# Performance work log

Hardware: AMD Instinct MI355X
Metric: run time of the kernel (lower is better)

The kernel has to match this reference:

```python
import jax, jax.numpy as jnp
import numpy as np

N = 1_000_000          # number of points
V = 65536              # number of voxels / groups (static stand-in for unique(coors))
IN_CH = 64             # 3 xyz + 61 extra features
HID = 64               # feat_channels = [64, 64]
REL_HID = 16           # rel_mlp_hidden_dims = [16]
XYZ_NORM = jnp.asarray([1.0, 1.0, 1.0], dtype=jnp.float32)
REL_DIST_SCALER = jnp.float32(1.0)


def setup_inputs() -> dict:
    key = jax.random.key(0)
    ks = jax.random.split(key, 10)

    def lin(k, i, o):
        return (jax.random.normal(k, (i, o), jnp.float32) / np.sqrt(i)).astype(jnp.float32)

    return {
        "points_xyzs": jax.random.normal(ks[0], (N, 3), jnp.float32),
        "points_feat": jax.random.normal(ks[1], (N, IN_CH - 3), jnp.float32),
        "f_cluster": jax.random.normal(ks[2], (N, 3), jnp.float32),
        "coors": jax.random.randint(ks[3], (N,), 0, V, jnp.int32),
        # rel_mlp: Linear(3,16)+BN+ReLU, Linear(16,64)+BN+ReLU (inference BN folded to scale/shift)
        "rel_w0": lin(ks[4], 3, REL_HID),
        "rel_g0": jnp.ones((REL_HID,), jnp.float32),
        "rel_b0": jnp.zeros((REL_HID,), jnp.float32),
        "rel_w1": lin(ks[5], REL_HID, IN_CH),
        "rel_g1": jnp.ones((IN_CH,), jnp.float32),
        "rel_b1": jnp.zeros((IN_CH,), jnp.float32),
        # vfe layer 0: Linear(64,64)+BN+ReLU;  vfe layer 1: Linear(128,64)+BN+ReLU (in_filters*=2 for i>0)
        "vfe_w0": lin(ks[6], IN_CH, HID),
        "vfe_g0": jnp.ones((HID,), jnp.float32),
        "vfe_b0": jnp.zeros((HID,), jnp.float32),
        "vfe_w1": lin(ks[7], 2 * HID, HID),
        "vfe_g1": jnp.ones((HID,), jnp.float32),
        "vfe_b1": jnp.zeros((HID,), jnp.float32),
    }


def _bn_relu(x, g, b):
    # inference BatchNorm1d folded into per-channel scale/shift, then ReLU
    return jax.nn.relu(x * g + b)


def _forward(points_xyzs, points_feat, f_cluster, coors,
             rel_w0, rel_g0, rel_b0, rel_w1, rel_g1, rel_b1,
             vfe_w0, vfe_g0, vfe_b0, vfe_w1, vfe_g1, vfe_b1):
    xyz = points_xyzs / XYZ_NORM                              # [N, 3]
    feats = jnp.concatenate([xyz, points_feat], axis=-1)      # [N, IN_CH]
    shortcut = feats
    fc = f_cluster / REL_DIST_SCALER                          # [N, 3]
    # relative-position MLP gating: features *= rel_mlp(f_cluster)
    h = _bn_relu(fc @ rel_w0, rel_g0, rel_b0)                 # [N, REL_HID]
    gate = _bn_relu(h @ rel_w1, rel_g1, rel_b1)               # [N, IN_CH]
    feats = feats * gate
    # VFE layer 0: per-point MLP -> voxel-wise scatter max -> gather back -> concat
    p0 = _bn_relu(feats @ vfe_w0, vfe_g0, vfe_b0)             # [N, HID]
    v0 = jax.ops.segment_max(p0, coors, num_segments=V)       # [V, HID]
    v0 = jnp.where(jnp.isfinite(v0), v0, jnp.float32(0.0))    # empty voxels -> 0
    feats = jnp.concatenate([p0, v0[coors]], axis=-1)         # [N, 2*HID]
    # VFE layer 1 (last): per-point MLP, plus residual shortcut (shapes match)
    p1 = _bn_relu(feats @ vfe_w1, vfe_g1, vfe_b1)             # [N, HID]
    return p1 + shortcut


def reference(points_xyzs, points_feat, f_cluster, coors,
              rel_w0, rel_g0, rel_b0, rel_w1, rel_g1, rel_b1,
              vfe_w0, vfe_g0, vfe_b0, vfe_w1, vfe_g1, vfe_b1):
    return _forward(points_xyzs, points_feat, f_cluster, coors,
                    rel_w0, rel_g0, rel_b0, rel_w1, rel_g1, rel_b1,
                    vfe_w0, vfe_g0, vfe_b0, vfe_w1, vfe_g1, vfe_b1)
```

## Files before the change

### kernel.cpp

```cpp
#include <hip/hip_runtime.h>
#include <hip/hip_bf16.h>


#define VVOX 65536

__global__ void __launch_bounds__(256)
sir_k1(const float* __restrict__ xyz,
       const float* __restrict__ pfeat,
       const float* __restrict__ fclu,
       const int* __restrict__ coors,
       const float* __restrict__ rw0,
       const float* __restrict__ rg0,
       const float* __restrict__ rb0,
       const float* __restrict__ rw1,
       const float* __restrict__ rg1,
       const float* __restrict__ rb1,
       const float* __restrict__ vw0,
       const float* __restrict__ vg0,
       const float* __restrict__ vb0,
       unsigned int* __restrict__ vmax,
       float* __restrict__ p0out,
       int npts)
{
    __shared__ float s_w0[48];
    __shared__ float s_b0[16];
    __shared__ float s_w1t[1024];
    __shared__ float s_b1[64];
    __shared__ float s_vw0[4096];
    __shared__ float s_vb0[64];

    const int t = threadIdx.x;
    for (int i = t; i < 48; i += 256) s_w0[i] = rw0[i] * rg0[i & 15];
    if (t < 16) s_b0[t] = rb0[t];
    for (int i = t; i < 1024; i += 256) {
        int k = i >> 4, j = i & 15;
        s_w1t[i] = rw1[j * 64 + k] * rg1[k];
    }
    if (t < 64) s_b1[t] = rb1[t];
    for (int i = t; i < 4096; i += 256) s_vw0[i] = vw0[i] * vg0[i & 63];
    if (t < 64) s_vb0[t] = vb0[t];
    __syncthreads();

    const int pt = blockIdx.x * 256 + t;
    if (pt >= npts) return;

    float f[64];
    {
        const float* xr = xyz + (size_t)pt * 3;
        f[0] = xr[0]; f[1] = xr[1]; f[2] = xr[2];
        const float* fr = pfeat + (size_t)pt * 61;
        #pragma unroll
        for (int k = 0; k < 61; ++k) f[3 + k] = fr[k];
    }

    const float* cr = fclu + (size_t)pt * 3;
    const float c0 = cr[0], c1 = cr[1], c2 = cr[2];
    float h[16];
    #pragma unroll
    for (int j = 0; j < 16; ++j) {
        float v = s_b0[j];
        v = fmaf(c0, s_w0[j], v);
        v = fmaf(c1, s_w0[16 + j], v);
        v = fmaf(c2, s_w0[32 + j], v);
        h[j] = fmaxf(v, 0.f);
    }

    float acc[64];
    #pragma unroll
    for (int c = 0; c < 64; ++c) acc[c] = s_vb0[c];

    for (int k = 0; k < 64; ++k) {
        float g = s_b1[k];
        const float* w1k = s_w1t + k * 16;
        #pragma unroll
        for (int j = 0; j < 16; ++j) g = fmaf(h[j], w1k[j], g);
        g = fmaxf(g, 0.f);
        const float gk = f[k] * g;
        const float* wk = s_vw0 + k * 64;
        #pragma unroll
        for (int c = 0; c < 64; ++c) acc[c] = fmaf(gk, wk[c], acc[c]);
    }

    const int vox = coors[pt];
    unsigned int* vrow = vmax + (size_t)vox * 64;
    const uint4* vrow4 = reinterpret_cast<const uint4*>(vrow);
    float4* orow = reinterpret_cast<float4*>(p0out + (size_t)pt * 64);
    #pragma unroll
    for (int q = 0; q < 16; ++q) {
        const uint4 cur = vrow4[q];
        float4 u;
        u.x = fmaxf(acc[q * 4 + 0], 0.f);
        u.y = fmaxf(acc[q * 4 + 1], 0.f);
        u.z = fmaxf(acc[q * 4 + 2], 0.f);
        u.w = fmaxf(acc[q * 4 + 3], 0.f);
        orow[q] = u;
        if (__float_as_uint(u.x) > cur.x) atomicMax(vrow + q * 4 + 0, __float_as_uint(u.x));
        if (__float_as_uint(u.y) > cur.y) atomicMax(vrow + q * 4 + 1, __float_as_uint(u.y));
        if (__float_as_uint(u.z) > cur.z) atomicMax(vrow + q * 4 + 2, __float_as_uint(u.z));
        if (__float_as_uint(u.w) > cur.w) atomicMax(vrow + q * 4 + 3, __float_as_uint(u.w));
    }
}

__global__ void __launch_bounds__(256)
sir_k2(const float* __restrict__ xyz,
       const float* __restrict__ pfeat,
       const int* __restrict__ coors,
       const float* __restrict__ vw1,
       const float* __restrict__ vg1,
       const float* __restrict__ vb1,
       const float* __restrict__ vmaxf,
       float* __restrict__ io,
       int npts)
{
    __shared__ float s_w[8192];
    __shared__ float s_b[64];
    const int t = threadIdx.x;
    for (int i = t; i < 8192; i += 256) s_w[i] = vw1[i] * vg1[i & 63];
    if (t < 64) s_b[t] = vb1[t];
    __syncthreads();

    const int pt = blockIdx.x * 256 + t;
    if (pt >= npts) return;

    float acc[64];
    #pragma unroll
    for (int c = 0; c < 64; ++c) acc[c] = s_b[c];

    const float4* prow = reinterpret_cast<const float4*>(io + (size_t)pt * 64);
    for (int q = 0; q < 16; ++q) {
        const float4 u = prow[q];
        const float pv[4] = { u.x, u.y, u.z, u.w };
        const float* wk = s_w + q * 4 * 64;
        #pragma unroll
        for (int i = 0; i < 4; ++i) {
            const float pk = pv[i];
            #pragma unroll
            for (int c = 0; c < 64; ++c) acc[c] = fmaf(pk, wk[i * 64 + c], acc[c]);
        }
    }

    const int vox = coors[pt];
    const float4* vrow = reinterpret_cast<const float4*>(vmaxf + (size_t)vox * 64);
    for (int q = 0; q < 16; ++q) {
        const float4 u = vrow[q];
        const float vv[4] = { u.x, u.y, u.z, u.w };
        const float* wk = s_w + (64 + q * 4) * 64;
        #pragma unroll
        for (int i = 0; i < 4; ++i) {
            const float vk = vv[i];
            #pragma unroll
            for (int c = 0; c < 64; ++c) acc[c] = fmaf(vk, wk[i * 64 + c], acc[c]);
        }
    }

    const float* xr = xyz + (size_t)pt * 3;
    const float* fr = pfeat + (size_t)pt * 61;
    float4* orow = reinterpret_cast<float4*>(io + (size_t)pt * 64);
    #pragma unroll
    for (int q = 0; q < 16; ++q) {
        float4 u;
        const int c = q * 4;
        const float s0 = (c + 0 < 3) ? xr[c + 0] : fr[c - 3];
        const float s1 = (c + 1 < 3) ? xr[c + 1] : fr[c - 2];
        const float s2 = (c + 2 < 3) ? xr[c + 2] : fr[c - 1];
        const float s3 = (c + 3 < 3) ? xr[c + 3] : fr[c + 0];
        u.x = fmaxf(acc[c + 0], 0.f) + s0;
        u.y = fmaxf(acc[c + 1], 0.f) + s1;
        u.z = fmaxf(acc[c + 2], 0.f) + s2;
        u.w = fmaxf(acc[c + 3], 0.f) + s3;
        orow[q] = u;
    }
}

extern "C" void kernel_launch(void* const* d_in, const int* in_sizes, int n_in,
                              void* d_out, int out_size, void* d_ws, size_t ws_size,
                              hipStream_t stream) {
    const float* xyz   = (const float*)d_in[0];
    const float* pfeat = (const float*)d_in[1];
    const float* fclu  = (const float*)d_in[2];
    const int*   coors = (const int*)d_in[3];
    const float* rw0 = (const float*)d_in[4];
    const float* rg0 = (const float*)d_in[5];
    const float* rb0 = (const float*)d_in[6];
    const float* rw1 = (const float*)d_in[7];
    const float* rg1 = (const float*)d_in[8];
    const float* rb1 = (const float*)d_in[9];
    const float* vw0 = (const float*)d_in[10];
    const float* vg0 = (const float*)d_in[11];
    const float* vb0 = (const float*)d_in[12];
    const float* vw1 = (const float*)d_in[13];
    const float* vg1 = (const float*)d_in[14];
    const float* vb1 = (const float*)d_in[15];

    float*        out  = (float*)d_out;
    unsigned int* vmax = (unsigned int*)d_ws;
    const int npts = in_sizes[3];
    const int blocks = (npts + 255) / 256;

    hipMemsetAsync(d_ws, 0, (size_t)VVOX * 64 * sizeof(float), stream);

    hipLaunchKernelGGL(sir_k1, dim3(blocks), dim3(256), 0, stream,
                       xyz, pfeat, fclu, coors,
                       rw0, rg0, rb0, rw1, rg1, rb1,
                       vw0, vg0, vb0, vmax, out, npts);

    hipLaunchKernelGGL(sir_k2, dim3(blocks), dim3(256), 0, stream,
                       xyz, pfeat, coors,
                       vw1, vg1, vb1, (const float*)d_ws, out, npts);
}
```

Baseline: 1.670 ms.

## Split gate and VFE0 GEMM kernels, register-block 4 points x 16 channels

The fused first kernel is split into two. One kernel computes the rel-MLP gated features and writes them into the output buffer. The second kernel runs the 64x64 projection plus the scatter-max, with each thread computing 4 points by 16 output channels and prefetching the next float4 of inputs. The second VFE kernel is restructured into the same 4x16 register tile. The aim is to cut per-thread register pressure from the 64-wide accumulator and feature arrays, and to reuse each shared-memory weight read across four points. In exchange the gated features make an extra round trip through global memory, and there is one more kernel launch.

```diff
diff --git a/kernel.cpp b/kernel.cpp
--- a/kernel.cpp
+++ b/kernel.cpp
@@ -1,57 +1,38 @@
 #include <hip/hip_runtime.h>
-#include <hip/hip_bf16.h>
 
 
 #define VVOX 65536
 
 __global__ void __launch_bounds__(256)
-sir_k1(const float* __restrict__ xyz,
-       const float* __restrict__ pfeat,
-       const float* __restrict__ fclu,
-       const int* __restrict__ coors,
-       const float* __restrict__ rw0,
-       const float* __restrict__ rg0,
-       const float* __restrict__ rb0,
-       const float* __restrict__ rw1,
-       const float* __restrict__ rg1,
-       const float* __restrict__ rb1,
-       const float* __restrict__ vw0,
-       const float* __restrict__ vg0,
-       const float* __restrict__ vb0,
-       unsigned int* __restrict__ vmax,
-       float* __restrict__ p0out,
-       int npts)
+sir_k1a(const float* __restrict__ xyz,
+        const float* __restrict__ pfeat,
+        const float* __restrict__ fclu,
+        const float* __restrict__ rw0,
+        const float* __restrict__ rg0,
+        const float* __restrict__ rb0,
+        const float* __restrict__ rw1,
+        const float* __restrict__ rg1,
+        const float* __restrict__ rb1,
+        float* __restrict__ G,
+        int npts)
 {
     __shared__ float s_w0[48];
     __shared__ float s_b0[16];
     __shared__ float s_w1t[1024];
     __shared__ float s_b1[64];
-    __shared__ float s_vw0[4096];
-    __shared__ float s_vb0[64];
 
     const int t = threadIdx.x;
-    for (int i = t; i < 48; i += 256) s_w0[i] = rw0[i] * rg0[i & 15];
+    if (t < 48) s_w0[t] = rw0[t] * rg0[t & 15];
     if (t < 16) s_b0[t] = rb0[t];
     for (int i = t; i < 1024; i += 256) {
         int k = i >> 4, j = i & 15;
         s_w1t[i] = rw1[j * 64 + k] * rg1[k];
     }
     if (t < 64) s_b1[t] = rb1[t];
-    for (int i = t; i < 4096; i += 256) s_vw0[i] = vw0[i] * vg0[i & 63];
-    if (t < 64) s_vb0[t] = vb0[t];
     __syncthreads();
 
     const int pt = blockIdx.x * 256 + t;
     if (pt >= npts) return;
-
-    float f[64];
-    {
-        const float* xr = xyz + (size_t)pt * 3;
-        f[0] = xr[0]; f[1] = xr[1]; f[2] = xr[2];
-        const float* fr = pfeat + (size_t)pt * 61;
-        #pragma unroll
-        for (int k = 0; k < 61; ++k) f[3 + k] = fr[k];
-    }
 
     const float* cr = fclu + (size_t)pt * 3;
     const float c0 = cr[0], c1 = cr[1], c2 = cr[2];
@@ -65,39 +46,120 @@
         h[j] = fmaxf(v, 0.f);
     }
 
-    float acc[64];
-    #pragma unroll
-    for (int c = 0; c < 64; ++c) acc[c] = s_vb0[c];
-
-    for (int k = 0; k < 64; ++k) {
-        float g = s_b1[k];
-        const float* w1k = s_w1t + k * 16;
-        #pragma unroll
-        for (int j = 0; j < 16; ++j) g = fmaf(h[j], w1k[j], g);
-        g = fmaxf(g, 0.f);
-        const float gk = f[k] * g;
-        const float* wk = s_vw0 + k * 64;
-        #pragma unroll
-        for (int c = 0; c < 64; ++c) acc[c] = fmaf(gk, wk[c], acc[c]);
-    }
-
-    const int vox = coors[pt];
-    unsigned int* vrow = vmax + (size_t)vox * 64;
-    const uint4* vrow4 = reinterpret_cast<const uint4*>(vrow);
-    float4* orow = reinterpret_cast<float4*>(p0out + (size_t)pt * 64);
-    #pragma unroll
-    for (int q = 0; q < 16; ++q) {
-        const uint4 cur = vrow4[q];
-        float4 u;
-        u.x = fmaxf(acc[q * 4 + 0], 0.f);
-        u.y = fmaxf(acc[q * 4 + 1], 0.f);
-        u.z = fmaxf(acc[q * 4 + 2], 0.f);
-        u.w = fmaxf(acc[q * 4 + 3], 0.f);
-        orow[q] = u;
-        if (__float_as_uint(u.x) > cur.x) atomicMax(vrow + q * 4 + 0, __float_as_uint(u.x));
-        if (__float_as_uint(u.y) > cur.y) atomicMax(vrow + q * 4 + 1, __float_as_uint(u.y));
-        if (__float_as_uint(u.z) > cur.z) atomicMax(vrow + q * 4 + 2, __float_as_uint(u.z));
-        if (__float_as_uint(u.w) > cur.w) atomicMax(vrow + q * 4 + 3, __float_as_uint(u.w));
+    const float* xr = xyz + (size_t)pt * 3;
+    const float* fr = pfeat + (size_t)pt * 61;
+    float4* Grow = reinterpret_cast<float4*>(G + (size_t)pt * 64);
+
+    #pragma unroll 4
+    for (int k4 = 0; k4 < 16; ++k4) {
+        float u[4];
+        #pragma unroll
+        for (int kk = 0; kk < 4; ++kk) {
+            const int k = k4 * 4 + kk;
+            const float* w1k = s_w1t + k * 16;
+            float g0 = s_b1[k], g1 = 0.f, g2 = 0.f, g3 = 0.f;
+            #pragma unroll
+            for (int j = 0; j < 4; ++j) {
+                g0 = fmaf(h[j],      w1k[j],      g0);
+                g1 = fmaf(h[4 + j],  w1k[4 + j],  g1);
+                g2 = fmaf(h[8 + j],  w1k[8 + j],  g2);
+                g3 = fmaf(h[12 + j], w1k[12 + j], g3);
+            }
+            const float g = fmaxf((g0 + g1) + (g2 + g3), 0.f);
+            const float fk = (k < 3) ? xr[k] : fr[k - 3];
+            u[kk] = fk * g;
+        }
+        float4 uu;
+        uu.x = u[0]; uu.y = u[1]; uu.z = u[2]; uu.w = u[3];
+        Grow[k4] = uu;
+    }
+}
+
+__global__ void __launch_bounds__(256)
+sir_k1b(const float* __restrict__ G,
+        const int* __restrict__ coors,
+        const float* __restrict__ vw0,
+        const float* __restrict__ vg0,
+        const float* __restrict__ vb0,
+        unsigned int* __restrict__ vmax,
+        float* __restrict__ p0out,
+        int npts)
+{
+    __shared__ float s_w[4096];
+    __shared__ float s_b[64];
+    const int t = threadIdx.x;
+    for (int i = t; i < 4096; i += 256) s_w[i] = vw0[i] * vg0[i & 63];
+    if (t < 64) s_b[t] = vb0[t];
+    __syncthreads();
+
+    const int cg = t & 3;
+    const int ps = t >> 2;
+    const int base = blockIdx.x * 256;
+
+    int p[4]; bool ok[4];
+    const float4* Gp[4];
+    #pragma unroll
+    for (int i = 0; i < 4; ++i) {
+        p[i] = base + ps + 64 * i;
+        ok[i] = p[i] < npts;
+        const int pc = ok[i] ? p[i] : 0;
+        Gp[i] = reinterpret_cast<const float4*>(G + (size_t)pc * 64);
+    }
+
+    float acc[4][16];
+    #pragma unroll
+    for (int i = 0; i < 4; ++i)
+        #pragma unroll
+        for (int c = 0; c < 16; ++c) acc[i][c] = s_b[cg * 16 + c];
+
+    float4 gv[4], gvn[4];
+    #pragma unroll
+    for (int i = 0; i < 4; ++i) gv[i] = Gp[i][0];
+
+    for (int k4 = 0; k4 < 16; ++k4) {
+        const int k4n = (k4 + 1) & 15;
+        #pragma unroll
+        for (int i = 0; i < 4; ++i) gvn[i] = Gp[i][k4n];
+        const float* wb = s_w + k4 * 256 + cg * 16;
+        #pragma unroll
+        for (int kk = 0; kk < 4; ++kk) {
+            const float* wr = wb + kk * 64;
+            #pragma unroll
+            for (int i = 0; i < 4; ++i) {
+                const float ga[4] = { gv[i].x, gv[i].y, gv[i].z, gv[i].w };
+                const float gk = ga[kk];
+                #pragma unroll
+                for (int c = 0; c < 16; ++c)
+                    acc[i][c] = fmaf(gk, wr[c], acc[i][c]);
+            }
+        }
+        #pragma unroll
+        for (int i = 0; i < 4; ++i) gv[i] = gvn[i];
+    }
+
+    __syncthreads();
+
+    #pragma unroll
+    for (int i = 0; i < 4; ++i) {
+        if (!ok[i]) continue;
+        const int vox = coors[p[i]];
+        unsigned int* vrow = vmax + (size_t)vox * 64 + cg * 16;
+        const uint4* vrow4 = reinterpret_cast<const uint4*>(vrow);
+        float4* orow = reinterpret_cast<float4*>(p0out + (size_t)p[i] * 64 + cg * 16);
+        #pragma unroll
+        for (int q = 0; q < 4; ++q) {
+            const uint4 cur = vrow4[q];
+            float4 u;
+            u.x = fmaxf(acc[i][q * 4 + 0], 0.f);
+            u.y = fmaxf(acc[i][q * 4 + 1], 0.f);
+            u.z = fmaxf(acc[i][q * 4 + 2], 0.f);
+            u.w = fmaxf(acc[i][q * 4 + 3], 0.f);
+            orow[q] = u;
+            if (__float_as_uint(u.x) > cur.x) atomicMax(vrow + q * 4 + 0, __float_as_uint(u.x));
+            if (__float_as_uint(u.y) > cur.y) atomicMax(vrow + q * 4 + 1, __float_as_uint(u.y));
+            if (__float_as_uint(u.z) > cur.z) atomicMax(vrow + q * 4 + 2, __float_as_uint(u.z));
+            if (__float_as_uint(u.w) > cur.w) atomicMax(vrow + q * 4 + 3, __float_as_uint(u.w));
+        }
     }
 }
 
@@ -119,56 +181,99 @@
     if (t < 64) s_b[t] = vb1[t];
     __syncthreads();
 
-    const int pt = blockIdx.x * 256 + t;
-    if (pt >= npts) return;
-
-    float acc[64];
-    #pragma unroll
-    for (int c = 0; c < 64; ++c) acc[c] = s_b[c];
-
-    const float4* prow = reinterpret_cast<const float4*>(io + (size_t)pt * 64);
-    for (int q = 0; q < 16; ++q) {
-        const float4 u = prow[q];
-        const float pv[4] = { u.x, u.y, u.z, u.w };
-        const float* wk = s_w + q * 4 * 64;
-        #pragma unroll
-        for (int i = 0; i < 4; ++i) {
-            const float pk = pv[i];
+    const int cg = t & 3;
+    const int ps = t >> 2;
+    const int base = blockIdx.x * 256;
+
+    int p[4]; bool ok[4];
+    const float4* prow[4];
+    const float4* vrow[4];
+    #pragma unroll
+    for (int i = 0; i < 4; ++i) {
+        p[i] = base + ps + 64 * i;
+        ok[i] = p[i] < npts;
+        const int pc = ok[i] ? p[i] : 0;
+        prow[i] = reinterpret_cast<const float4*>(io + (size_t)pc * 64);
+        const int vox = coors[pc];
+        vrow[i] = reinterpret_cast<const float4*>(vmaxf + (size_t)vox * 64);
+    }
+
+    float acc[4][16];
+    #pragma unroll
+    for (int i = 0; i < 4; ++i)
+        #pragma unroll
+        for (int c = 0; c < 16; ++c) acc[i][c] = s_b[cg * 16 + c];
+
+    float4 gv[4], gvn[4];
+
+    #pragma unroll
+    for (int i = 0; i < 4; ++i) gv[i] = prow[i][0];
+    for (int k4 = 0; k4 < 16; ++k4) {
+        const int k4n = (k4 + 1) & 15;
+        #pragma unroll
+        for (int i = 0; i < 4; ++i) gvn[i] = prow[i][k4n];
+        const float* wb = s_w + k4 * 256 + cg * 16;
+        #pragma unroll
+        for (int kk = 0; kk < 4; ++kk) {
+            const float* wr = wb + kk * 64;
             #pragma unroll
-            for (int c = 0; c < 64; ++c) acc[c] = fmaf(pk, wk[i * 64 + c], acc[c]);
-        }
-    }
-
-    const int vox = coors[pt];
-    const float4* vrow = reinterpret_cast<const float4*>(vmaxf + (size_t)vox * 64);
-    for (int q = 0; q < 16; ++q) {
-        const float4 u = vrow[q];
-        const float vv[4] = { u.x, u.y, u.z, u.w };
-        const float* wk = s_w + (64 + q * 4) * 64;
-        #pragma unroll
-        for (int i = 0; i < 4; ++i) {
-            const float vk = vv[i];
+            for (int i = 0; i < 4; ++i) {
+                const float ga[4] = { gv[i].x, gv[i].y, gv[i].z, gv[i].w };
+                const float gk = ga[kk];
+                #pragma unroll
+                for (int c = 0; c < 16; ++c)
+                    acc[i][c] = fmaf(gk, wr[c], acc[i][c]);
+            }
+        }
+        #pragma unroll
+        for (int i = 0; i < 4; ++i) gv[i] = gvn[i];
+    }
+
+    #pragma unroll
+    for (int i = 0; i < 4; ++i) gv[i] = vrow[i][0];
+    for (int k4 = 0; k4 < 16; ++k4) {
+        const int k4n = (k4 + 1) & 15;
+        #pragma unroll
+        for (int i = 0; i < 4; ++i) gvn[i] = vrow[i][k4n];
+        const float* wb = s_w + 4096 + k4 * 256 + cg * 16;
+        #pragma unroll
+        for (int kk = 0; kk < 4; ++kk) {
+            const float* wr = wb + kk * 64;
             #pragma unroll
-            for (int c = 0; c < 64; ++c) acc[c] = fmaf(vk, wk[i * 64 + c], acc[c]);
-        }
-    }
-
-    const float* xr = xyz + (size_t)pt * 3;
-    const float* fr = pfeat + (size_t)pt * 61;
-    float4* orow = reinterpret_cast<float4*>(io + (size_t)pt * 64);
-    #pragma unroll
-    for (int q = 0; q < 16; ++q) {
-        float4 u;
-        const int c = q * 4;
-        const float s0 = (c + 0 < 3) ? xr[c + 0] : fr[c - 3];
-        const float s1 = (c + 1 < 3) ? xr[c + 1] : fr[c - 2];
-        const float s2 = (c + 2 < 3) ? xr[c + 2] : fr[c - 1];
-        const float s3 = (c + 3 < 3) ? xr[c + 3] : fr[c + 0];
-        u.x = fmaxf(acc[c + 0], 0.f) + s0;
-        u.y = fmaxf(acc[c + 1], 0.f) + s1;
-        u.z = fmaxf(acc[c + 2], 0.f) + s2;
-        u.w = fmaxf(acc[c + 3], 0.f) + s3;
-        orow[q] = u;
+            for (int i = 0; i < 4; ++i) {
+                const float ga[4] = { gv[i].x, gv[i].y, gv[i].z, gv[i].w };
+                const float gk = ga[kk];
+                #pragma unroll
+                for (int c = 0; c < 16; ++c)
+                    acc[i][c] = fmaf(gk, wr[c], acc[i][c]);
+            }
+        }
+        #pragma unroll
+        for (int i = 0; i < 4; ++i) gv[i] = gvn[i];
+    }
+
+    __syncthreads();
+
+    #pragma unroll
+    for (int i = 0; i < 4; ++i) {
+        if (!ok[i]) continue;
+        const float* xr = xyz + (size_t)p[i] * 3;
+        const float* fr = pfeat + (size_t)p[i] * 61;
+        float4* orow = reinterpret_cast<float4*>(io + (size_t)p[i] * 64 + cg * 16);
+        #pragma unroll
+        for (int q = 0; q < 4; ++q) {
+            const int c = cg * 16 + q * 4;
+            const float s0 = (c + 0 < 3) ? xr[c + 0] : fr[c - 3];
+            const float s1 = (c + 1 < 3) ? xr[c + 1] : fr[c - 2];
+            const float s2 = (c + 2 < 3) ? xr[c + 2] : fr[c - 1];
+            const float s3 = (c + 3 < 3) ? xr[c + 3] : fr[c + 0];
+            float4 u;
+            u.x = fmaxf(acc[i][q * 4 + 0], 0.f) + s0;
+            u.y = fmaxf(acc[i][q * 4 + 1], 0.f) + s1;
+            u.z = fmaxf(acc[i][q * 4 + 2], 0.f) + s2;
+            u.w = fmaxf(acc[i][q * 4 + 3], 0.f) + s3;
+            orow[q] = u;
+        }
     }
 }
 
@@ -199,10 +304,13 @@
 
     hipMemsetAsync(d_ws, 0, (size_t)VVOX * 64 * sizeof(float), stream);
 
-    hipLaunchKernelGGL(sir_k1, dim3(blocks), dim3(256), 0, stream,
-                       xyz, pfeat, fclu, coors,
+    hipLaunchKernelGGL(sir_k1a, dim3(blocks), dim3(256), 0, stream,
+                       xyz, pfeat, fclu,
                        rw0, rg0, rb0, rw1, rg1, rb1,
-                       vw0, vg0, vb0, vmax, out, npts);
+                       out, npts);
+
+    hipLaunchKernelGGL(sir_k1b, dim3(blocks), dim3(256), 0, stream,
+                       out, coors, vw0, vg0, vb0, vmax, out, npts);
 
     hipLaunchKernelGGL(sir_k2, dim3(blocks), dim3(256), 0, stream,
                        xyz, pfeat, coors,
```

Result: slower. 1.945 ms (+16.5%).
